# Optimization experiments

Hardware: AMD Instinct MI355X
Metric: run time of the kernel (lower is better)

## Reference

```python
import jax, jax.numpy as jnp
import numpy as np

D_MODEL = 1024
N_HEADS = 16
HEAD_DIM = D_MODEL // N_HEADS


def setup_inputs() -> dict:
    key = jax.random.key(0)
    kx, kq, kk, kv, ko = jax.random.split(key, 5)
    B, T = 2, 2048
    # nn.Linear(d_model, d_model, bias=False) weights, stored as [out, in] like torch
    s = 1.0 / np.sqrt(D_MODEL)
    x = jax.random.normal(kx, (B, T, D_MODEL), dtype=jnp.float32)
    Wq = jax.random.uniform(kq, (D_MODEL, D_MODEL), minval=-s, maxval=s, dtype=jnp.float32)
    Wk = jax.random.uniform(kk, (D_MODEL, D_MODEL), minval=-s, maxval=s, dtype=jnp.float32)
    Wv = jax.random.uniform(kv, (D_MODEL, D_MODEL), minval=-s, maxval=s, dtype=jnp.float32)
    Wo = jax.random.uniform(ko, (D_MODEL, D_MODEL), minval=-s, maxval=s, dtype=jnp.float32)
    return {"x": x, "Wq": Wq, "Wk": Wk, "Wv": Wv, "Wo": Wo}


def reference(x, Wq, Wk, Wv, Wo):
    B, T, C = x.shape
    H, Dh = N_HEADS, HEAD_DIM
    # projections (torch Linear: x @ W.T)
    q = (x @ Wq.T).reshape(B, T, H, Dh).transpose(0, 2, 1, 3)  # [B,H,T,Dh]
    k = (x @ Wk.T).reshape(B, T, H, Dh).transpose(0, 2, 1, 3)
    v = (x @ Wv.T).reshape(B, T, H, Dh).transpose(0, 2, 1, 3)
    scores = jnp.einsum('bhqd,bhkd->bhqk', q, k) / jnp.sqrt(jnp.float32(Dh))
    causal = jnp.tril(jnp.ones((T, T), dtype=bool))  # [T,T]
    scores = jnp.where(causal[None, None], scores, -jnp.inf)
    attn = jax.nn.softmax(scores, axis=-1)
    out = jnp.einsum('bhqk,bhkd->bhqd', attn, v)  # [B,H,T,Dh]
    out = out.transpose(0, 2, 1, 3).reshape(B, T, C)
    return out @ Wo.T
```

## Files before the change

### kernel.cpp

```cpp
#include <hip/hip_runtime.h>
#include <hip/hip_bf16.h>

#define BB 2
#define TT 2048
#define CC 1024
#define HH 16
#define DH 64

typedef __attribute__((ext_vector_type(8))) short bf16x8;
typedef __attribute__((ext_vector_type(4))) float f32x4;
using bf16 = __hip_bfloat16;

union cvt8u { bf16x8 v; bf16 b[8]; };

__device__ __forceinline__ bf16x8 load8(const bf16* p) {
    return *reinterpret_cast<const bf16x8*>(p);
}

__device__ __forceinline__ bf16x8 cvt8f(const float* p) {
    const float4 a = *reinterpret_cast<const float4*>(p);
    const float4 c = *reinterpret_cast<const float4*>(p + 4);
    cvt8u u;
    u.b[0] = __float2bfloat16(a.x); u.b[1] = __float2bfloat16(a.y);
    u.b[2] = __float2bfloat16(a.z); u.b[3] = __float2bfloat16(a.w);
    u.b[4] = __float2bfloat16(c.x); u.b[5] = __float2bfloat16(c.y);
    u.b[6] = __float2bfloat16(c.z); u.b[7] = __float2bfloat16(c.w);
    return u.v;
}

__device__ __forceinline__ f32x4 mfma16(bf16x8 a, bf16x8 b, f32x4 c) {
    return __builtin_amdgcn_mfma_f32_16x16x32_bf16(a, b, c, 0, 0, 0);
}

__device__ __forceinline__ void gload_lds16(const bf16* g, bf16* l) {
    __builtin_amdgcn_global_load_lds(
        (const __attribute__((address_space(1))) void*)g,
        (__attribute__((address_space(3))) void*)l, 16, 0, 0);
}

#define QSCALE (0.125f * 1.44269504088896f)

__global__ __launch_bounds__(256) void cvt_x(const float* __restrict__ in,
                                             bf16* __restrict__ out) {
    const int i = blockIdx.x * 256 + threadIdx.x;
    *(reinterpret_cast<bf16x8*>(out) + i) = cvt8f(in + (size_t)i * 8);
}

__global__ __launch_bounds__(256) void cvt4_w(const float* __restrict__ w0,
                                              const float* __restrict__ w1,
                                              const float* __restrict__ w2,
                                              const float* __restrict__ w3,
                                              bf16* __restrict__ out) {
    const float* in = (blockIdx.y == 0) ? w0 : (blockIdx.y == 1) ? w1
                    : (blockIdx.y == 2) ? w2 : w3;
    const int i = blockIdx.x * 256 + threadIdx.x;
    bf16* o = out + (size_t)blockIdx.y * CC * CC;
    *(reinterpret_cast<bf16x8*>(o) + i) = cvt8f(in + (size_t)i * 8);
}

template <int MODE>
__global__ __launch_bounds__(256) void gemm3(const bf16* __restrict__ A,
                                             const bf16* __restrict__ B,
                                             bf16* __restrict__ oq,
                                             bf16* __restrict__ ok,
                                             bf16* __restrict__ ov,
                                             float* __restrict__ outf) {
    __shared__ __align__(16) bf16 As[128 * 32];
    __shared__ __align__(16) bf16 Bs[128 * 32];
    const int lane = threadIdx.x & 63;
    const int wv = threadIdx.x >> 6;
    const int l15 = lane & 15;
    const int g = lane >> 4;
    const int m0 = blockIdx.x * 128;
    const int n0 = blockIdx.y * 128;

    const int srow = wv * 16 + (lane >> 2);
    const int skg = (lane & 3) * 8;
    const bf16* gA0 = A + (size_t)(m0 + srow) * CC + skg;
    const bf16* gA1 = A + (size_t)(m0 + 64 + srow) * CC + skg;
    const bf16* gB0 = B + (size_t)(n0 + srow) * CC + skg;
    const bf16* gB1 = B + (size_t)(n0 + 64 + srow) * CC + skg;
    bf16* lA0 = As + wv * 512;
    bf16* lA1 = As + 2048 + wv * 512;
    bf16* lB0 = Bs + wv * 512;
    bf16* lB1 = Bs + 2048 + wv * 512;

    const int mw = (wv >> 1) * 64;
    const int nw = (wv & 1) * 64;

    f32x4 acc[4][4] = {};

    for (int kk = 0; kk < CC; kk += 32) {
        __syncthreads();
        gload_lds16(gA0 + kk, lA0);
        gload_lds16(gA1 + kk, lA1);
        gload_lds16(gB0 + kk, lB0);
        gload_lds16(gB1 + kk, lB1);
        __syncthreads();

        bf16x8 af[4], wf[4];
#pragma unroll
        for (int mi = 0; mi < 4; mi++)
            af[mi] = load8(As + (mw + mi * 16 + l15) * 32 + g * 8);
#pragma unroll
        for (int ni = 0; ni < 4; ni++)
            wf[ni] = load8(Bs + (nw + ni * 16 + l15) * 32 + g * 8);
#pragma unroll
        for (int mi = 0; mi < 4; mi++)
#pragma unroll
            for (int ni = 0; ni < 4; ni++)
                acc[mi][ni] = mfma16(af[mi], wf[ni], acc[mi][ni]);
    }

#pragma unroll
    for (int mi = 0; mi < 4; mi++) {
#pragma unroll
        for (int ni = 0; ni < 4; ni++) {
            const int n = n0 + nw + ni * 16 + l15;
#pragma unroll
            for (int r = 0; r < 4; r++) {
                const int m = m0 + mw + mi * 16 + g * 4 + r;
                const float v = acc[mi][ni][r];
                if (MODE == 1) {
                    outf[(size_t)m * CC + n] = v;
                } else {
                    const int b = m >> 11, t = m & (TT - 1);
                    const int mat = n >> 10, nn = n & 1023;
                    const int h = nn >> 6, d = nn & 63;
                    if (mat == 0) {
                        oq[((size_t)((b * HH + h) * TT + t) << 6) + d] = __float2bfloat16(v * QSCALE);
                    } else if (mat == 1) {
                        ok[((size_t)((b * HH + h) * TT + t) << 6) + d] = __float2bfloat16(v);
                    } else {
                        ov[(size_t)((b * HH + h) * DH + d) * TT + t] = __float2bfloat16(v);
                    }
                }
            }
        }
    }
}

template <int MODE>
__global__ __launch_bounds__(256) void gemm2(const bf16* __restrict__ A,
                                             const float* __restrict__ W0,
                                             const float* __restrict__ W1,
                                             const float* __restrict__ W2,
                                             bf16* __restrict__ oq,
                                             bf16* __restrict__ ok,
                                             bf16* __restrict__ ov,
                                             float* __restrict__ outf) {
    const int lane = threadIdx.x & 63;
    const int wv = threadIdx.x >> 6;
    const int l15 = lane & 15;
    const int g = lane >> 4;
    const int mw = blockIdx.x * 128 + (wv >> 1) * 64;
    const int nw = blockIdx.y * 128 + (wv & 1) * 64;

    f32x4 acc[4][4] = {};

    const bf16* ap[4];
#pragma unroll
    for (int mi = 0; mi < 4; mi++)
        ap[mi] = A + (size_t)(mw + mi * 16 + l15) * CC + g * 8;

    const float* wfp[4];
#pragma unroll
    for (int ni = 0; ni < 4; ni++) {
        const int nt = nw + ni * 16;
        const float* base = (MODE == 1) ? W0
                          : (nt < 1024) ? W0 : (nt < 2048) ? W1 : W2;
        wfp[ni] = base + (size_t)((nt & 1023) + l15) * CC + g * 8;
    }

#pragma unroll 2
    for (int kk = 0; kk < CC; kk += 32) {
        bf16x8 af[4], wf[4];
#pragma unroll
        for (int mi = 0; mi < 4; mi++) af[mi] = load8(ap[mi] + kk);
#pragma unroll
        for (int ni = 0; ni < 4; ni++) wf[ni] = cvt8f(wfp[ni] + kk);
#pragma unroll
        for (int mi = 0; mi < 4; mi++)
#pragma unroll
            for (int ni = 0; ni < 4; ni++)
                acc[mi][ni] = mfma16(af[mi], wf[ni], acc[mi][ni]);
    }

#pragma unroll
    for (int mi = 0; mi < 4; mi++) {
#pragma unroll
        for (int ni = 0; ni < 4; ni++) {
            const int n = nw + ni * 16 + l15;
#pragma unroll
            for (int r = 0; r < 4; r++) {
                const int m = mw + mi * 16 + g * 4 + r;
                const float v = acc[mi][ni][r];
                if (MODE == 1) {
                    outf[(size_t)m * CC + n] = v;
                } else {
                    const int b = m >> 11, t = m & (TT - 1);
                    const int mat = n >> 10, nn = n & 1023;
                    const int h = nn >> 6, d = nn & 63;
                    if (mat == 0) {
                        oq[((size_t)((b * HH + h) * TT + t) << 6) + d] = __float2bfloat16(v * QSCALE);
                    } else if (mat == 1) {
                        ok[((size_t)((b * HH + h) * TT + t) << 6) + d] = __float2bfloat16(v);
                    } else {
                        ov[(size_t)((b * HH + h) * DH + d) * TT + t] = __float2bfloat16(v);
                    }
                }
            }
        }
    }
}

__global__ __launch_bounds__(128, 2) void attn_v8(const bf16* __restrict__ Q,
                                                  const bf16* __restrict__ K,
                                                  const bf16* __restrict__ Vt,
                                                  bf16* __restrict__ out) {
    __shared__ __align__(16) char smem[18432];
    bf16* const pbase = reinterpret_cast<bf16*>(smem);
    float* const o_cmb = reinterpret_cast<float*>(smem);
    float* const l_cmb = reinterpret_cast<float*>(smem + 8192);

    const int lane = threadIdx.x & 63;
    const int wv = threadIdx.x >> 6;
    const int l15 = lane & 15;
    const int g = lane >> 4;

    const int bid = blockIdx.x;
    const int xcd = bid & 7;
    const int idx = bid >> 3;
    const int bh = xcd * 4 + (idx >> 6);
    const int c = idx & 63;

    const int qbA = c * 16;
    const int qbB = (127 - c) * 16;
    const int nkbA = (c >> 2) + 1;
    const int nkbB = ((127 - c) >> 2) + 1;

    const bf16* Qh = Q + (size_t)bh * TT * DH;
    const bf16* Kh = K + (size_t)bh * TT * DH;
    const bf16* Vh = Vt + (size_t)bh * DH * TT;

    const bf16x8 qa0 = load8(Qh + (size_t)(qbA + l15) * DH + g * 8);
    const bf16x8 qa1 = load8(Qh + (size_t)(qbA + l15) * DH + 32 + g * 8);
    const bf16x8 qb0 = load8(Qh + (size_t)(qbB + l15) * DH + g * 8);
    const bf16x8 qb1 = load8(Qh + (size_t)(qbB + l15) * DH + 32 + g * 8);

    f32x4 oA[4] = {}, oB[4] = {};
    float lA[4] = {0.0f, 0.0f, 0.0f, 0.0f};
    float lB[4] = {0.0f, 0.0f, 0.0f, 0.0f};

    bf16* const pw = pbase + wv * 2 * 2 * 1152;

    bf16x8 kf0[4], kf1[4];
#pragma unroll
    for (int j = 0; j < 4; j++) {
        kf0[j] = load8(Kh + (size_t)(wv * 64 + j * 16 + l15) * DH + g * 8);
        kf1[j] = load8(Kh + (size_t)(wv * 64 + j * 16 + l15) * DH + 32 + g * 8);
    }

    bf16x8 vf0[4], vf1[4];
    int par = 0;
    bool haveP = false, prevA = false;

    for (int kb = wv; kb < nkbB; kb += 2) {
        const int k0 = kb * 64;
        const bool actA = (kb < nkbA);

        f32x4 SA[4] = {}, SB[4] = {};
        if (actA) {
#pragma unroll
            for (int j = 0; j < 4; j++) {
                SA[j] = mfma16(qa0, kf0[j], SA[j]);
                SA[j] = mfma16(qa1, kf1[j], SA[j]);
            }
        }
#pragma unroll
        for (int j = 0; j < 4; j++) {
            SB[j] = mfma16(qb0, kf0[j], SB[j]);
            SB[j] = mfma16(qb1, kf1[j], SB[j]);
        }

        if (haveP) {
            asm volatile("s_waitcnt lgkmcnt(0)" ::: "memory");
            const bf16* rB = pw + ((par ^ 1) * 2 + 1) * 1152;
            const bf16x8 pb0 = load8(rB + l15 * 72 + g * 8);
            const bf16x8 pb1 = load8(rB + l15 * 72 + 32 + g * 8);
#pragma unroll
            for (int dt = 0; dt < 4; dt++) {
                oB[dt] = mfma16(pb0, vf0[dt], oB[dt]);
                oB[dt] = mfma16(pb1, vf1[dt], oB[dt]);
            }
            if (prevA) {
                const bf16* rA = pw + ((par ^ 1) * 2 + 0) * 1152;
                const bf16x8 pa0 = load8(rA + l15 * 72 + g * 8);
                const bf16x8 pa1 = load8(rA + l15 * 72 + 32 + g * 8);
#pragma unroll
                for (int dt = 0; dt < 4; dt++) {
                    oA[dt] = mfma16(pa0, vf0[dt], oA[dt]);
                    oA[dt] = mfma16(pa1, vf1[dt], oA[dt]);
                }
            }
        }

#pragma unroll
        for (int dt = 0; dt < 4; dt++) {
            vf0[dt] = load8(Vh + (size_t)(dt * 16 + l15) * TT + k0 + g * 8);
            vf1[dt] = load8(Vh + (size_t)(dt * 16 + l15) * TT + k0 + 32 + g * 8);
        }

        if (kb + 2 < nkbB) {
            const int kn = k0 + 128;
#pragma unroll
            for (int j = 0; j < 4; j++) {
                kf0[j] = load8(Kh + (size_t)(kn + j * 16 + l15) * DH + g * 8);
                kf1[j] = load8(Kh + (size_t)(kn + j * 16 + l15) * DH + 32 + g * 8);
            }
        }

        if (actA && kb == nkbA - 1) {
#pragma unroll
            for (int j = 0; j < 4; j++)
#pragma unroll
                for (int r = 0; r < 4; r++)
                    if (k0 + j * 16 + l15 > qbA + g * 4 + r) SA[j][r] = -1e30f;
        }
        if (kb == nkbB - 1) {
#pragma unroll
            for (int j = 0; j < 4; j++)
#pragma unroll
                for (int r = 0; r < 4; r++)
                    if (k0 + j * 16 + l15 > qbB + g * 4 + r) SB[j][r] = -1e30f;
        }

        if (actA) {
#pragma unroll
            for (int r = 0; r < 4; r++)
#pragma unroll
                for (int j = 0; j < 4; j++) {
                    SA[j][r] = exp2f(SA[j][r]);
                    lA[r] += SA[j][r];
                }
        }
#pragma unroll
        for (int r = 0; r < 4; r++)
#pragma unroll
            for (int j = 0; j < 4; j++) {
                SB[j][r] = exp2f(SB[j][r]);
                lB[r] += SB[j][r];
            }

        bf16* wA = pw + (par * 2 + 0) * 1152;
        bf16* wB = pw + (par * 2 + 1) * 1152;
        if (actA) {
#pragma unroll
            for (int j = 0; j < 4; j++)
#pragma unroll
                for (int r = 0; r < 4; r++)
                    wA[(g * 4 + r) * 72 + j * 16 + l15] = __float2bfloat16(SA[j][r]);
        }
#pragma unroll
        for (int j = 0; j < 4; j++)
#pragma unroll
            for (int r = 0; r < 4; r++)
                wB[(g * 4 + r) * 72 + j * 16 + l15] = __float2bfloat16(SB[j][r]);

        par ^= 1;
        haveP = true;
        prevA = actA;
    }

    {
        asm volatile("s_waitcnt lgkmcnt(0)" ::: "memory");
        const bf16* rB = pw + ((par ^ 1) * 2 + 1) * 1152;
        const bf16x8 pb0 = load8(rB + l15 * 72 + g * 8);
        const bf16x8 pb1 = load8(rB + l15 * 72 + 32 + g * 8);
#pragma unroll
        for (int dt = 0; dt < 4; dt++) {
            oB[dt] = mfma16(pb0, vf0[dt], oB[dt]);
            oB[dt] = mfma16(pb1, vf1[dt], oB[dt]);
        }
        if (prevA) {
            const bf16* rA = pw + ((par ^ 1) * 2 + 0) * 1152;
            const bf16x8 pa0 = load8(rA + l15 * 72 + g * 8);
            const bf16x8 pa1 = load8(rA + l15 * 72 + 32 + g * 8);
#pragma unroll
            for (int dt = 0; dt < 4; dt++) {
                oA[dt] = mfma16(pa0, vf0[dt], oA[dt]);
                oA[dt] = mfma16(pa1, vf1[dt], oA[dt]);
            }
        }
    }

#pragma unroll
    for (int xm = 1; xm < 16; xm <<= 1) {
#pragma unroll
        for (int r = 0; r < 4; r++) {
            lA[r] += __shfl_xor(lA[r], xm);
            lB[r] += __shfl_xor(lB[r], xm);
        }
    }

    __syncthreads();

    if (wv == 1) {
#pragma unroll
        for (int dt = 0; dt < 4; dt++) {
            *reinterpret_cast<f32x4*>(&o_cmb[((0 * 4 + dt) * 64 + lane) * 4]) = oA[dt];
            *reinterpret_cast<f32x4*>(&o_cmb[((1 * 4 + dt) * 64 + lane) * 4]) = oB[dt];
        }
        if (l15 == 0) {
#pragma unroll
            for (int r = 0; r < 4; r++) {
                l_cmb[0 * 16 + g * 4 + r] = lA[r];
                l_cmb[1 * 16 + g * 4 + r] = lB[r];
            }
        }
    }
    __syncthreads();
    if (wv == 1) return;

#pragma unroll
    for (int dt = 0; dt < 4; dt++) {
        oA[dt] += *reinterpret_cast<const f32x4*>(&o_cmb[((0 * 4 + dt) * 64 + lane) * 4]);
        oB[dt] += *reinterpret_cast<const f32x4*>(&o_cmb[((1 * 4 + dt) * 64 + lane) * 4]);
    }
#pragma unroll
    for (int r = 0; r < 4; r++) {
        lA[r] += l_cmb[0 * 16 + g * 4 + r];
        lB[r] += l_cmb[1 * 16 + g * 4 + r];
    }

    const int b = bh >> 4, h = bh & 15;
#pragma unroll
    for (int r = 0; r < 4; r++) {
        const float invA = 1.0f / lA[r];
        const float invB = 1.0f / lB[r];
        const int tA = qbA + g * 4 + r;
        const int tB = qbB + g * 4 + r;
        bf16* opA = out + (size_t)(b * TT + tA) * CC + h * DH;
        bf16* opB = out + (size_t)(b * TT + tB) * CC + h * DH;
#pragma unroll
        for (int dt = 0; dt < 4; dt++) {
            opA[dt * 16 + l15] = __float2bfloat16(oA[dt][r] * invA);
            opB[dt * 16 + l15] = __float2bfloat16(oB[dt][r] * invB);
        }
    }
}

extern "C" void kernel_launch(void* const* d_in, const int* in_sizes, int n_in,
                              void* d_out, int out_size, void* d_ws, size_t ws_size,
                              hipStream_t stream) {
    const float* x  = (const float*)d_in[0];
    const float* Wq = (const float*)d_in[1];
    const float* Wk = (const float*)d_in[2];
    const float* Wv = (const float*)d_in[3];
    const float* Wo = (const float*)d_in[4];
    float* out = (float*)d_out;

    const size_t per = (size_t)BB * HH * TT * DH;
    bf16* Qws  = (bf16*)d_ws;
    bf16* Kws  = Qws + per;
    bf16* Vtws = Kws + per;
    bf16* xbf  = Vtws + per;
    bf16* attn = xbf;
    bf16* Wball = attn + per;
    const bool full = ws_size >= 5 * per * sizeof(bf16);

    const dim3 blk(256);
    cvt_x<<<dim3(2048), blk, 0, stream>>>(x, xbf);

    if (full) {
        cvt4_w<<<dim3(512, 4), blk, 0, stream>>>(Wq, Wk, Wv, Wo, Wball);
        gemm3<0><<<dim3(32, 24), blk, 0, stream>>>(
            xbf, Wball, Qws, Kws, Vtws, nullptr);
    } else {
        gemm2<0><<<dim3(32, 24), blk, 0, stream>>>(
            xbf, Wq, Wk, Wv, Qws, Kws, Vtws, nullptr);
    }

    attn_v8<<<dim3(2048), dim3(128), 0, stream>>>(Qws, Kws, Vtws, attn);

    if (full) {
        gemm3<1><<<dim3(32, 8), blk, 0, stream>>>(
            attn, Wball + (size_t)3 * CC * CC, nullptr, nullptr, nullptr, out);
    } else {
        gemm2<1><<<dim3(32, 8), blk, 0, stream>>>(
            attn, Wo, nullptr, nullptr, nullptr, nullptr, nullptr, out);
    }
}
```

Baseline: 240.8 us.

## Widen attention key blocks to 128 and drop the P double-buffer pipeline

The attention kernel now processes 128-key blocks per wave instead of 64, so each wave runs half as many loop iterations and holds twice as many K fragments and four V fragment sets in registers. The previous software pipeline, which deferred the PV MFMA by one iteration using double-buffered P tiles in LDS, is replaced by a single P buffer that is written and then read back within the same iteration. The intent is to cut per-iteration loop and synchronisation overhead. In exchange, register pressure rises sharply and the overlap between V loads and PV compute is lost, and the coarser causal granularity adds masked work on the diagonal.

```diff
diff --git a/kernel.cpp b/kernel.cpp
--- a/kernel.cpp
+++ b/kernel.cpp
@@ -214,11 +214,11 @@
     }
 }
 
-__global__ __launch_bounds__(128, 2) void attn_v8(const bf16* __restrict__ Q,
+__global__ __launch_bounds__(128, 2) void attn_v9(const bf16* __restrict__ Q,
                                                   const bf16* __restrict__ K,
                                                   const bf16* __restrict__ Vt,
                                                   bf16* __restrict__ out) {
-    __shared__ __align__(16) char smem[18432];
+    __shared__ __align__(16) char smem[17408];
     bf16* const pbase = reinterpret_cast<bf16*>(smem);
     float* const o_cmb = reinterpret_cast<float*>(smem);
     float* const l_cmb = reinterpret_cast<float*>(smem + 8192);
@@ -236,8 +236,8 @@
 
     const int qbA = c * 16;
     const int qbB = (127 - c) * 16;
-    const int nkbA = (c >> 2) + 1;
-    const int nkbB = ((127 - c) >> 2) + 1;
+    const int nkA = (c >> 3) + 1;
+    const int nkB = ((127 - c) >> 3) + 1;
 
     const bf16* Qh = Q + (size_t)bh * TT * DH;
     const bf16* Kh = K + (size_t)bh * TT * DH;
@@ -252,84 +252,60 @@
     float lA[4] = {0.0f, 0.0f, 0.0f, 0.0f};
     float lB[4] = {0.0f, 0.0f, 0.0f, 0.0f};
 
-    bf16* const pw = pbase + wv * 2 * 2 * 1152;
-
-    bf16x8 kf0[4], kf1[4];
-#pragma unroll
-    for (int j = 0; j < 4; j++) {
-        kf0[j] = load8(Kh + (size_t)(wv * 64 + j * 16 + l15) * DH + g * 8);
-        kf1[j] = load8(Kh + (size_t)(wv * 64 + j * 16 + l15) * DH + 32 + g * 8);
-    }
-
-    bf16x8 vf0[4], vf1[4];
-    int par = 0;
-    bool haveP = false, prevA = false;
-
-    for (int kb = wv; kb < nkbB; kb += 2) {
-        const int k0 = kb * 64;
-        const bool actA = (kb < nkbA);
-
-        f32x4 SA[4] = {}, SB[4] = {};
+    bf16* const plA = pbase + (wv * 2 + 0) * 2176;
+    bf16* const plB = pbase + (wv * 2 + 1) * 2176;
+
+    bf16x8 kf0[8], kf1[8];
+#pragma unroll
+    for (int j = 0; j < 8; j++) {
+        kf0[j] = load8(Kh + (size_t)(wv * 128 + j * 16 + l15) * DH + g * 8);
+        kf1[j] = load8(Kh + (size_t)(wv * 128 + j * 16 + l15) * DH + 32 + g * 8);
+    }
+
+    for (int kb = wv; kb < nkB; kb += 2) {
+        const int k0 = kb * 128;
+        const bool actA = (kb < nkA);
+
+        f32x4 SA[8] = {}, SB[8] = {};
         if (actA) {
 #pragma unroll
-            for (int j = 0; j < 4; j++) {
+            for (int j = 0; j < 8; j++) {
                 SA[j] = mfma16(qa0, kf0[j], SA[j]);
                 SA[j] = mfma16(qa1, kf1[j], SA[j]);
             }
         }
 #pragma unroll
-        for (int j = 0; j < 4; j++) {
+        for (int j = 0; j < 8; j++) {
             SB[j] = mfma16(qb0, kf0[j], SB[j]);
             SB[j] = mfma16(qb1, kf1[j], SB[j]);
         }
 
-        if (haveP) {
-            asm volatile("s_waitcnt lgkmcnt(0)" ::: "memory");
-            const bf16* rB = pw + ((par ^ 1) * 2 + 1) * 1152;
-            const bf16x8 pb0 = load8(rB + l15 * 72 + g * 8);
-            const bf16x8 pb1 = load8(rB + l15 * 72 + 32 + g * 8);
-#pragma unroll
-            for (int dt = 0; dt < 4; dt++) {
-                oB[dt] = mfma16(pb0, vf0[dt], oB[dt]);
-                oB[dt] = mfma16(pb1, vf1[dt], oB[dt]);
-            }
-            if (prevA) {
-                const bf16* rA = pw + ((par ^ 1) * 2 + 0) * 1152;
-                const bf16x8 pa0 = load8(rA + l15 * 72 + g * 8);
-                const bf16x8 pa1 = load8(rA + l15 * 72 + 32 + g * 8);
-#pragma unroll
-                for (int dt = 0; dt < 4; dt++) {
-                    oA[dt] = mfma16(pa0, vf0[dt], oA[dt]);
-                    oA[dt] = mfma16(pa1, vf1[dt], oA[dt]);
-                }
-            }
-        }
-
-#pragma unroll
-        for (int dt = 0; dt < 4; dt++) {
-            vf0[dt] = load8(Vh + (size_t)(dt * 16 + l15) * TT + k0 + g * 8);
-            vf1[dt] = load8(Vh + (size_t)(dt * 16 + l15) * TT + k0 + 32 + g * 8);
-        }
-
-        if (kb + 2 < nkbB) {
-            const int kn = k0 + 128;
-#pragma unroll
-            for (int j = 0; j < 4; j++) {
+        bf16x8 vf[4][4];
+#pragma unroll
+        for (int dt = 0; dt < 4; dt++)
+#pragma unroll
+            for (int ks = 0; ks < 4; ks++)
+                vf[ks][dt] = load8(Vh + (size_t)(dt * 16 + l15) * TT + k0 + ks * 32 + g * 8);
+
+        if (kb + 2 < nkB) {
+            const int kn = k0 + 256;
+#pragma unroll
+            for (int j = 0; j < 8; j++) {
                 kf0[j] = load8(Kh + (size_t)(kn + j * 16 + l15) * DH + g * 8);
                 kf1[j] = load8(Kh + (size_t)(kn + j * 16 + l15) * DH + 32 + g * 8);
             }
         }
 
-        if (actA && kb == nkbA - 1) {
-#pragma unroll
-            for (int j = 0; j < 4; j++)
+        if (actA && kb == nkA - 1) {
+#pragma unroll
+            for (int j = 0; j < 8; j++)
 #pragma unroll
                 for (int r = 0; r < 4; r++)
                     if (k0 + j * 16 + l15 > qbA + g * 4 + r) SA[j][r] = -1e30f;
         }
-        if (kb == nkbB - 1) {
-#pragma unroll
-            for (int j = 0; j < 4; j++)
+        if (kb == nkB - 1) {
+#pragma unroll
+            for (int j = 0; j < 8; j++)
 #pragma unroll
                 for (int r = 0; r < 4; r++)
                     if (k0 + j * 16 + l15 > qbB + g * 4 + r) SB[j][r] = -1e30f;
@@ -339,7 +315,7 @@
 #pragma unroll
             for (int r = 0; r < 4; r++)
 #pragma unroll
-                for (int j = 0; j < 4; j++) {
+                for (int j = 0; j < 8; j++) {
                     SA[j][r] = exp2f(SA[j][r]);
                     lA[r] += SA[j][r];
                 }
@@ -347,50 +323,44 @@
 #pragma unroll
         for (int r = 0; r < 4; r++)
 #pragma unroll
-            for (int j = 0; j < 4; j++) {
+            for (int j = 0; j < 8; j++) {
                 SB[j][r] = exp2f(SB[j][r]);
                 lB[r] += SB[j][r];
             }
 
-        bf16* wA = pw + (par * 2 + 0) * 1152;
-        bf16* wB = pw + (par * 2 + 1) * 1152;
         if (actA) {
 #pragma unroll
-            for (int j = 0; j < 4; j++)
+            for (int j = 0; j < 8; j++)
 #pragma unroll
                 for (int r = 0; r < 4; r++)
-                    wA[(g * 4 + r) * 72 + j * 16 + l15] = __float2bfloat16(SA[j][r]);
-        }
-#pragma unroll
-        for (int j = 0; j < 4; j++)
+                    plA[(g * 4 + r) * 136 + j * 16 + l15] = __float2bfloat16(SA[j][r]);
+        }
+#pragma unroll
+        for (int j = 0; j < 8; j++)
 #pragma unroll
             for (int r = 0; r < 4; r++)
-                wB[(g * 4 + r) * 72 + j * 16 + l15] = __float2bfloat16(SB[j][r]);
-
-        par ^= 1;
-        haveP = true;
-        prevA = actA;
-    }
-
-    {
+                plB[(g * 4 + r) * 136 + j * 16 + l15] = __float2bfloat16(SB[j][r]);
         asm volatile("s_waitcnt lgkmcnt(0)" ::: "memory");
-        const bf16* rB = pw + ((par ^ 1) * 2 + 1) * 1152;
-        const bf16x8 pb0 = load8(rB + l15 * 72 + g * 8);
-        const bf16x8 pb1 = load8(rB + l15 * 72 + 32 + g * 8);
-#pragma unroll
-        for (int dt = 0; dt < 4; dt++) {
-            oB[dt] = mfma16(pb0, vf0[dt], oB[dt]);
-            oB[dt] = mfma16(pb1, vf1[dt], oB[dt]);
-        }
-        if (prevA) {
-            const bf16* rA = pw + ((par ^ 1) * 2 + 0) * 1152;
-            const bf16x8 pa0 = load8(rA + l15 * 72 + g * 8);
-            const bf16x8 pa1 = load8(rA + l15 * 72 + 32 + g * 8);
-#pragma unroll
-            for (int dt = 0; dt < 4; dt++) {
-                oA[dt] = mfma16(pa0, vf0[dt], oA[dt]);
-                oA[dt] = mfma16(pa1, vf1[dt], oA[dt]);
-            }
+
+        bf16x8 pB[4];
+#pragma unroll
+        for (int ks = 0; ks < 4; ks++)
+            pB[ks] = load8(plB + l15 * 136 + ks * 32 + g * 8);
+#pragma unroll
+        for (int dt = 0; dt < 4; dt++)
+#pragma unroll
+            for (int ks = 0; ks < 4; ks++)
+                oB[dt] = mfma16(pB[ks], vf[ks][dt], oB[dt]);
+        if (actA) {
+            bf16x8 pA[4];
+#pragma unroll
+            for (int ks = 0; ks < 4; ks++)
+                pA[ks] = load8(plA + l15 * 136 + ks * 32 + g * 8);
+#pragma unroll
+            for (int dt = 0; dt < 4; dt++)
+#pragma unroll
+                for (int ks = 0; ks < 4; ks++)
+                    oA[dt] = mfma16(pA[ks], vf[ks][dt], oA[dt]);
         }
     }
 
@@ -481,7 +451,7 @@
             xbf, Wq, Wk, Wv, Qws, Kws, Vtws, nullptr);
     }
 
-    attn_v8<<<dim3(2048), dim3(128), 0, stream>>>(Qws, Kws, Vtws, attn);
+    attn_v9<<<dim3(2048), dim3(128), 0, stream>>>(Qws, Kws, Vtws, attn);
 
     if (full) {
         gemm3<1><<<dim3(32, 8), blk, 0, stream>>>(
```

After: 276.0 us. +14.6%, slower.
